# Performance work log

Measured on AMD Instinct MI355X. Metric: run time of the kernel, lower is better.

The kernel has to match this reference:

```python
import jax, jax.numpy as jnp
import numpy as np

NEG_SLOPE = 0.2  # PyG GATConv default negative_slope


def gat_conv(x, src, dst, W, a_src, a_dst, b, concat):
    # x: [N, F_in]; src/dst: [E] edge endpoints (edge j->i means src=j, dst=i)
    N = x.shape[0]
    H, C = a_src.shape
    xp = (x @ W).reshape(N, H, C)                      # per-head projection
    al_s = jnp.einsum('nhc,hc->nh', xp, a_src)          # source attention logits
    al_d = jnp.einsum('nhc,hc->nh', xp, a_dst)          # destination attention logits
    e = jax.nn.leaky_relu(al_s[src] + al_d[dst], NEG_SLOPE)   # [E, H]
    # segment softmax over incoming edges of each destination node
    m = jax.ops.segment_max(e, dst, num_segments=N)     # [N, H]
    m = jnp.where(jnp.isfinite(m), m, jnp.zeros_like(m))
    ex = jnp.exp(e - m[dst])
    den = jax.ops.segment_sum(ex, dst, num_segments=N)  # [N, H]
    alpha = ex / (den[dst] + 1e-16)                     # [E, H]
    out = jax.ops.segment_sum(xp[src] * alpha[:, :, None], dst, num_segments=N)  # [N,H,C]
    out = out.reshape(N, H * C) if concat else out.mean(axis=1)
    return out + b


def setup_inputs() -> dict:
    key = jax.random.key(0)
    ks = jax.random.split(key, 9)
    N, E, F_in, H, C = 50000, 1600000, 128, 4, 32
    x = jax.random.normal(ks[0], (N, F_in), dtype=jnp.float32)
    edge_index = jax.random.randint(ks[1], (2, E), 0, N, dtype=jnp.int64)
    s1 = 1.0 / np.sqrt(F_in)
    s2 = 1.0 / np.sqrt(H * C)
    return {
        'x': x,
        'edge_index': edge_index,
        'W1': jax.random.normal(ks[2], (F_in, H * C), dtype=jnp.float32) * s1,
        'a_src1': jax.random.normal(ks[3], (H, C), dtype=jnp.float32) * s1,
        'a_dst1': jax.random.normal(ks[4], (H, C), dtype=jnp.float32) * s1,
        'b1': jnp.zeros((H * C,), dtype=jnp.float32),
        'W2': jax.random.normal(ks[5], (H * C, C), dtype=jnp.float32) * s2,
        'a_src2': jax.random.normal(ks[6], (1, C), dtype=jnp.float32) * s2,
        'a_dst2': jax.random.normal(ks[7], (1, C), dtype=jnp.float32) * s2,
        'b2': jnp.zeros((C,), dtype=jnp.float32),
    }


def reference(x, edge_index, W1, a_src1, a_dst1, b1, W2, a_src2, a_dst2, b2):
    N = x.shape[0]
    loops = jnp.arange(N, dtype=edge_index.dtype)
    src = jnp.concatenate([edge_index[0], loops])   # PyG default add_self_loops=True
    dst = jnp.concatenate([edge_index[1], loops])
    h = gat_conv(x, src, dst, W1, a_src1, a_dst1, b1, concat=True)
    h = jax.nn.elu(h)
    out = gat_conv(h, src, dst, W2, a_src2, a_dst2, b2, concat=False)
    return out
```

## Files before the change

### kernel.cpp

```cpp
#include <hip/hip_runtime.h>
#include <hip/hip_fp16.h>

#define NEG_SLOPE 0.2f
#define CAP 128
#define NB  64
#define GAB 192

typedef __half half_t;

__device__ __forceinline__ float lrelu(float x) { return x >= 0.f ? x : NEG_SLOPE * x; }

__device__ __forceinline__ unsigned int f2h2(float a, float b) {
    union { unsigned int u; __half2 h; } v; v.h = __floats2half2_rn(a, b);
    return v.u;
}

__device__ __forceinline__ void fma8h(const uint4& v, float w, float* a) {
    const __half* hp = (const __half*)&v;
    #pragma unroll
    for (int j = 0; j < 8; ++j) a[j] = fmaf(w, __half2float(hp[j]), a[j]);
}

__device__ __forceinline__ bool edge_is64(const int* __restrict__ ei, int E) {
    int t = threadIdx.x & 63;
    int idx = 2 * t + 1; if (idx >= 2 * E) idx = 2 * E - 1;
    unsigned long long b = __ballot(ei[idx] != 0);
    return b == 0ULL;
}

__device__ __forceinline__ void load_edge(const int* __restrict__ ei, int E, int i,
                                          bool is64, int& s, int& d) {
    if (i < E) {
        if (is64) { const long long* e = (const long long*)ei; s = (int)e[i]; d = (int)e[E + i]; }
        else      { s = ei[i]; d = ei[E + i]; }
    } else { s = d = i - E; }
}

__global__ __launch_bounds__(256) void gemm1cnt_kernel(const float* __restrict__ x,
        const float* __restrict__ W1, const float* __restrict__ a_src,
        const float* __restrict__ a_dst, half_t* __restrict__ xp1h,
        float* __restrict__ al_s, float* __restrict__ al_d,
        const int* __restrict__ ei, int* __restrict__ partials,
        int N, int E, int shift, int G1) {
    __shared__ __align__(16) float xst[64 * 128];
    __shared__ __align__(16) float ws[64 * 128];
    int t = threadIdx.x;
    if (blockIdx.x >= G1) {
        int* cnts = (int*)xst;
        int b2 = blockIdx.x - G1;
        if (t < NB) cnts[t] = 0;
        bool is64 = edge_is64(ei, E);
        __syncthreads();
        int tot = E + N;
        for (int i = b2 * 256 + t; i < tot; i += GAB * 256) {
            int s, d; load_edge(ei, E, i, is64, s, d);
            atomicAdd(&cnts[d >> shift], 1);
        }
        __syncthreads();
        if (t < NB) partials[b2 * NB + t] = cnts[t];
        return;
    }
    int row0 = blockIdx.x * 128;
    int cg = t & 15, rg = t >> 4;
    float acc[8][8] = {};
    for (int chunk = 0; chunk < 2; ++chunk) {
        __syncthreads();
        int c0 = chunk * 64;
        #pragma unroll
        for (int ii = 0; ii < 8; ++ii) {
            int idx = t + 256 * ii;
            int r = idx >> 4, kq = idx & 15;
            int n = row0 + r;
            float4 v = make_float4(0.f, 0.f, 0.f, 0.f);
            if (n < N) v = *(const float4*)&x[(size_t)n * 128 + c0 + kq * 4];
            float vv[4] = {v.x, v.y, v.z, v.w};
            #pragma unroll
            for (int j = 0; j < 4; ++j) {
                int k = kq * 4 + j;
                xst[k * 128 + (((r >> 2) ^ (k & 31)) << 2) + (r & 3)] = vv[j];
            }
        }
        #pragma unroll
        for (int ii = 0; ii < 8; ++ii) {
            int idx = t + 256 * ii;
            int k = idx >> 5, cq = idx & 31;
            *(float4*)&ws[k * 128 + cq * 4] =
                *(const float4*)&W1[(size_t)(c0 + k) * 128 + cq * 4];
        }
        __syncthreads();
        int g0 = rg * 2, g1 = rg * 2 + 1;
        #pragma unroll 4
        for (int k = 0; k < 64; ++k) {
            int kb = k & 31;
            float4 xv0 = *(const float4*)&xst[k * 128 + ((g0 ^ kb) << 2)];
            float4 xv1 = *(const float4*)&xst[k * 128 + ((g1 ^ kb) << 2)];
            float4 wv0 = *(const float4*)&ws[k * 128 + cg * 8];
            float4 wv1 = *(const float4*)&ws[k * 128 + cg * 8 + 4];
            float xr[8] = {xv0.x, xv0.y, xv0.z, xv0.w, xv1.x, xv1.y, xv1.z, xv1.w};
            float wr[8] = {wv0.x, wv0.y, wv0.z, wv0.w, wv1.x, wv1.y, wv1.z, wv1.w};
            #pragma unroll
            for (int r = 0; r < 8; ++r)
                #pragma unroll
                for (int c = 0; c < 8; ++c)
                    acc[r][c] = fmaf(xr[r], wr[c], acc[r][c]);
        }
    }
    #pragma unroll
    for (int r = 0; r < 8; ++r) {
        int n = row0 + rg * 8 + r;
        if (n < N) {
            uint4 u = make_uint4(f2h2(acc[r][0], acc[r][1]), f2h2(acc[r][2], acc[r][3]),
                                 f2h2(acc[r][4], acc[r][5]), f2h2(acc[r][6], acc[r][7]));
            *(uint4*)&xp1h[(size_t)n * 128 + cg * 8] = u;
        }
    }
    float ps[8], pd[8];
    #pragma unroll
    for (int r = 0; r < 8; ++r) {
        float s = 0.f, dd = 0.f;
        #pragma unroll
        for (int c = 0; c < 8; ++c) {
            s  = fmaf(acc[r][c], a_src[cg * 8 + c], s);
            dd = fmaf(acc[r][c], a_dst[cg * 8 + c], dd);
        }
        ps[r] = s; pd[r] = dd;
    }
    #pragma unroll
    for (int m = 1; m < 4; m <<= 1) {
        #pragma unroll
        for (int r = 0; r < 8; ++r) { ps[r] += __shfl_xor(ps[r], m); pd[r] += __shfl_xor(pd[r], m); }
    }
    if ((cg & 3) == 0) {
        int head = cg >> 2;
        #pragma unroll
        for (int r = 0; r < 8; ++r) {
            int n = row0 + rg * 8 + r;
            if (n < N) { al_s[n * 4 + head] = ps[r]; al_d[n * 4 + head] = pd[r]; }
        }
    }
}

__global__ __launch_bounds__(256) void k_scan(int* __restrict__ partials,
                                              int* __restrict__ bin_base) {
    __shared__ int lp[GAB * NB];
    __shared__ int tot[NB], base[NB];
    int t = threadIdx.x;
    for (int i = t; i < GAB * NB; i += 256) lp[i] = partials[i];
    __syncthreads();
    if (t < NB) {
        int run = 0;
        for (int b = 0; b < GAB; ++b) { int v = lp[b * NB + t]; lp[b * NB + t] = run; run += v; }
        tot[t] = run;
    }
    __syncthreads();
    if (t == 0) {
        int run = 0;
        for (int i = 0; i < NB; ++i) { base[i] = run; run += tot[i]; }
    }
    __syncthreads();
    if (t < NB) bin_base[t] = base[t];
    if (t == 0) bin_base[NB] = base[NB - 1] + tot[NB - 1];
    for (int i = t; i < GAB * NB; i += 256) partials[i] = lp[i] + base[i & (NB - 1)];
}

__global__ __launch_bounds__(256) void k_bin(const int* __restrict__ ei,
        int E, int N, int shift, const int* __restrict__ offsets, int* __restrict__ binned) {
    __shared__ int cur[NB];
    int t = threadIdx.x, b = blockIdx.x;
    if (t < NB) cur[t] = offsets[b * NB + t];
    bool is64 = edge_is64(ei, E);
    int mask = (1 << shift) - 1;
    __syncthreads();
    int tot = E + N;
    for (int i = b * 256 + t; i < tot; i += GAB * 256) {
        int s, d; load_edge(ei, E, i, is64, s, d);
        int pos = atomicAdd(&cur[d >> shift], 1);
        binned[pos] = ((d & mask) << 16) | s;
    }
}

__global__ __launch_bounds__(1024) void k_part(const int* __restrict__ binned,
        const int* __restrict__ bin_base, int* __restrict__ off, int* __restrict__ csr,
        int N, int shift) {
    __shared__ int cnt_loc[1024];
    __shared__ int scan_loc[1024];
    __shared__ int wsum[16];
    int b = blockIdx.x, t = threadIdx.x;
    int base = b << shift;
    int span = 1 << shift;
    int lo = bin_base[b], hi = bin_base[b + 1];
    if (t < span) cnt_loc[t] = 0;
    __syncthreads();
    for (int i = lo + t; i < hi; i += 1024)
        atomicAdd(&cnt_loc[binned[i] >> 16], 1);
    __syncthreads();
    int v = (t < span) ? cnt_loc[t] : 0;
    int lane = t & 63, w = t >> 6;
    int incl = v;
    #pragma unroll
    for (int m = 1; m < 64; m <<= 1) {
        int u = __shfl_up(incl, m);
        if (lane >= m) incl += u;
    }
    if (lane == 63) wsum[w] = incl;
    __syncthreads();
    if (t == 0) {
        int run = 0;
        #pragma unroll
        for (int i2 = 0; i2 < 16; ++i2) { int s2 = wsum[i2]; wsum[i2] = run; run += s2; }
    }
    __syncthreads();
    int excl = incl - v + wsum[w];
    if (t < span) { scan_loc[t] = lo + excl; off[base + t] = lo + excl; }
    __syncthreads();
    if (t < span) cnt_loc[t] = 0;
    __syncthreads();
    for (int i = lo + t; i < hi; i += 1024) {
        int e = binned[i];
        int r = e >> 16;
        int pos = scan_loc[r] + atomicAdd(&cnt_loc[r], 1);
        csr[pos] = e & 0xFFFF;
    }
}

__global__ __launch_bounds__(256) void edge1_kernel(const int* __restrict__ off,
        const int* __restrict__ csr, const float* __restrict__ al_s,
        const float* __restrict__ al_d, const half_t* __restrict__ xp1h,
        const float* __restrict__ b1, half_t* __restrict__ h1h, int N) {
    __shared__ int   srcs[4][CAP];
    __shared__ float ew[4][CAP * 4];
    int t = threadIdx.x;
    int wid = t >> 6, lane = t & 63;
    int d = blockIdx.x * 4 + wid;
    if (d >= N) return;
    int o0 = off[d], o1 = off[d + 1];
    int deg = o1 - o0; if (deg > CAP) deg = CAP;
    float4 ad = *(const float4*)&al_d[d * 4];
    float4 ex0 = make_float4(0.f, 0.f, 0.f, 0.f);
    float4 ex1 = make_float4(0.f, 0.f, 0.f, 0.f);
    if (lane < deg) {
        int s = csr[o0 + lane];
        srcs[wid][lane] = s;
        float4 as = *(const float4*)&al_s[s * 4];
        ex0.x = __expf(lrelu(as.x + ad.x));
        ex0.y = __expf(lrelu(as.y + ad.y));
        ex0.z = __expf(lrelu(as.z + ad.z));
        ex0.w = __expf(lrelu(as.w + ad.w));
    }
    if (lane + 64 < deg) {
        int s = csr[o0 + lane + 64];
        srcs[wid][lane + 64] = s;
        float4 as = *(const float4*)&al_s[s * 4];
        ex1.x = __expf(lrelu(as.x + ad.x));
        ex1.y = __expf(lrelu(as.y + ad.y));
        ex1.z = __expf(lrelu(as.z + ad.z));
        ex1.w = __expf(lrelu(as.w + ad.w));
    }
    float4 r = make_float4(ex0.x + ex1.x, ex0.y + ex1.y, ex0.z + ex1.z, ex0.w + ex1.w);
    #pragma unroll
    for (int m = 1; m < 64; m <<= 1) {
        r.x += __shfl_xor(r.x, m); r.y += __shfl_xor(r.y, m);
        r.z += __shfl_xor(r.z, m); r.w += __shfl_xor(r.w, m);
    }
    float4 ri = make_float4(1.f / (r.x + 1e-16f), 1.f / (r.y + 1e-16f),
                            1.f / (r.z + 1e-16f), 1.f / (r.w + 1e-16f));
    if (lane < deg)
        *(float4*)&ew[wid][lane * 4] =
            make_float4(ex0.x * ri.x, ex0.y * ri.y, ex0.z * ri.z, ex0.w * ri.w);
    if (lane + 64 < deg)
        *(float4*)&ew[wid][(lane + 64) * 4] =
            make_float4(ex1.x * ri.x, ex1.y * ri.y, ex1.z * ri.z, ex1.w * ri.w);
    int q = lane & 15, p = lane >> 4, h = q >> 2;
    float a[8] = {};
    const uint4* xr = (const uint4*)xp1h;
    for (int ib = p; ib < deg; ib += 16) {
        int i1 = ib + 4, i2 = ib + 8, i3 = ib + 12;
        bool c1 = i1 < deg, c2 = i2 < deg, c3 = i3 < deg;
        float w0 = ew[wid][ib * 4 + h];
        uint4 v0 = xr[(size_t)srcs[wid][ib] * 16 + q];
        float w1, w2, w3;
        uint4 v1, v2, v3;
        if (c1) { w1 = ew[wid][i1 * 4 + h]; v1 = xr[(size_t)srcs[wid][i1] * 16 + q]; }
        if (c2) { w2 = ew[wid][i2 * 4 + h]; v2 = xr[(size_t)srcs[wid][i2] * 16 + q]; }
        if (c3) { w3 = ew[wid][i3 * 4 + h]; v3 = xr[(size_t)srcs[wid][i3] * 16 + q]; }
        fma8h(v0, w0, a);
        if (c1) fma8h(v1, w1, a);
        if (c2) fma8h(v2, w2, a);
        if (c3) fma8h(v3, w3, a);
    }
    #pragma unroll
    for (int j = 0; j < 8; ++j) {
        a[j] += __shfl_xor(a[j], 16);
        a[j] += __shfl_xor(a[j], 32);
    }
    if (p == 0) {
        float4 b0 = *(const float4*)&b1[q * 8];
        float4 b4 = *(const float4*)&b1[q * 8 + 4];
        float v0 = a[0] + b0.x, v1 = a[1] + b0.y, v2 = a[2] + b0.z, v3 = a[3] + b0.w;
        float v4 = a[4] + b4.x, v5 = a[5] + b4.y, v6 = a[6] + b4.z, v7 = a[7] + b4.w;
        v0 = v0 > 0.f ? v0 : expm1f(v0);
        v1 = v1 > 0.f ? v1 : expm1f(v1);
        v2 = v2 > 0.f ? v2 : expm1f(v2);
        v3 = v3 > 0.f ? v3 : expm1f(v3);
        v4 = v4 > 0.f ? v4 : expm1f(v4);
        v5 = v5 > 0.f ? v5 : expm1f(v5);
        v6 = v6 > 0.f ? v6 : expm1f(v6);
        v7 = v7 > 0.f ? v7 : expm1f(v7);
        uint4 u = make_uint4(f2h2(v0, v1), f2h2(v2, v3), f2h2(v4, v5), f2h2(v6, v7));
        *(uint4*)&h1h[(size_t)d * 128 + q * 8] = u;
    }
}

__global__ __launch_bounds__(256) void gemm2l_kernel(const half_t* __restrict__ h1h,
        const float* __restrict__ W2, const float* __restrict__ a_s2,
        const float* __restrict__ a_d2, half_t* __restrict__ xp2h,
        float* __restrict__ al_s2, float* __restrict__ al_d2, int N) {
    __shared__ __align__(16) float w2s[128 * 32];
    int t = threadIdx.x;
    #pragma unroll
    for (int ii = 0; ii < 4; ++ii)
        ((float4*)w2s)[t + 256 * ii] = ((const float4*)W2)[t + 256 * ii];
    if (blockIdx.x == 0 && t < 2)
        ((uint4*)(xp2h + (size_t)N * 32))[t] = make_uint4(0, 0, 0, 0);
    __syncthreads();
    int n = blockIdx.x * 64 + (t >> 2), sub = t & 3;
    if (n >= N) return;
    const uint4* hr = (const uint4*)(h1h + (size_t)n * 128);
    float acc[8] = {};
    #pragma unroll 2
    for (int kq = 0; kq < 16; ++kq) {
        uint4 hv = hr[kq];
        const __half* hp = (const __half*)&hv;
        #pragma unroll
        for (int jj = 0; jj < 8; ++jj) {
            float h = __half2float(hp[jj]);
            int k = kq * 8 + jj;
            float4 wa = *(const float4*)&w2s[k * 32 + sub * 8];
            float4 wb = *(const float4*)&w2s[k * 32 + sub * 8 + 4];
            acc[0] = fmaf(h, wa.x, acc[0]); acc[1] = fmaf(h, wa.y, acc[1]);
            acc[2] = fmaf(h, wa.z, acc[2]); acc[3] = fmaf(h, wa.w, acc[3]);
            acc[4] = fmaf(h, wb.x, acc[4]); acc[5] = fmaf(h, wb.y, acc[5]);
            acc[6] = fmaf(h, wb.z, acc[6]); acc[7] = fmaf(h, wb.w, acc[7]);
        }
    }
    uint4 u = make_uint4(f2h2(acc[0], acc[1]), f2h2(acc[2], acc[3]),
                         f2h2(acc[4], acc[5]), f2h2(acc[6], acc[7]));
    *(uint4*)&xp2h[(size_t)n * 32 + sub * 8] = u;
    float ps = 0.f, pd = 0.f;
    #pragma unroll
    for (int c = 0; c < 8; ++c) {
        ps = fmaf(acc[c], a_s2[sub * 8 + c], ps);
        pd = fmaf(acc[c], a_d2[sub * 8 + c], pd);
    }
    ps += __shfl_xor(ps, 1); ps += __shfl_xor(ps, 2);
    pd += __shfl_xor(pd, 1); pd += __shfl_xor(pd, 2);
    if (sub == 0) { al_s2[n] = ps; al_d2[n] = pd; }
}

__global__ __launch_bounds__(256) void edge2_kernel(const int* __restrict__ off,
        const int* __restrict__ csr, const float* __restrict__ al_s,
        const float* __restrict__ al_d, const half_t* __restrict__ xp2h,
        const float* __restrict__ b2v, float* __restrict__ out, int N) {
    __shared__ int   srcs[4][CAP];
    __shared__ float ew[4][CAP];
    int t = threadIdx.x;
    int wid = t >> 6, lane = t & 63;
    int d = blockIdx.x * 4 + wid;
    if (d >= N) return;
    int o0 = off[d], o1 = off[d + 1];
    int deg = o1 - o0; if (deg > CAP) deg = CAP;
    float adv = al_d[d];
    float ex0 = 0.f, ex1 = 0.f;
    if (lane < deg) {
        int s = csr[o0 + lane];
        srcs[wid][lane] = s;
        ex0 = __expf(lrelu(al_s[s] + adv));
    }
    if (lane + 64 < deg) {
        int s = csr[o0 + lane + 64];
        srcs[wid][lane + 64] = s;
        ex1 = __expf(lrelu(al_s[s] + adv));
    }
    float r = ex0 + ex1;
    #pragma unroll
    for (int m = 1; m < 64; m <<= 1) r += __shfl_xor(r, m);
    float rinv = 1.f / (r + 1e-16f);
    if (lane < deg)      ew[wid][lane]      = ex0 * rinv;
    if (lane + 64 < deg) ew[wid][lane + 64] = ex1 * rinv;
    int q = lane & 3, p = lane >> 2;
    float a[8] = {};
    const uint4* xr = (const uint4*)xp2h;
    for (int ib = p; ib < deg; ib += 64) {
        int i1 = ib + 16, i2 = ib + 32, i3 = ib + 48;
        bool c1 = i1 < deg, c2 = i2 < deg, c3 = i3 < deg;
        float w0 = ew[wid][ib];
        uint4 v0 = xr[(size_t)srcs[wid][ib] * 4 + q];
        float w1, w2, w3;
        uint4 v1, v2, v3;
        if (c1) { w1 = ew[wid][i1]; v1 = xr[(size_t)srcs[wid][i1] * 4 + q]; }
        if (c2) { w2 = ew[wid][i2]; v2 = xr[(size_t)srcs[wid][i2] * 4 + q]; }
        if (c3) { w3 = ew[wid][i3]; v3 = xr[(size_t)srcs[wid][i3] * 4 + q]; }
        fma8h(v0, w0, a);
        if (c1) fma8h(v1, w1, a);
        if (c2) fma8h(v2, w2, a);
        if (c3) fma8h(v3, w3, a);
    }
    #pragma unroll
    for (int j = 0; j < 8; ++j) {
        a[j] += __shfl_xor(a[j], 4);
        a[j] += __shfl_xor(a[j], 8);
        a[j] += __shfl_xor(a[j], 16);
        a[j] += __shfl_xor(a[j], 32);
    }
    if (p == 0) {
        float4 b0 = *(const float4*)&b2v[q * 8];
        float4 b4 = *(const float4*)&b2v[q * 8 + 4];
        float4 o0v = make_float4(a[0] + b0.x, a[1] + b0.y, a[2] + b0.z, a[3] + b0.w);
        float4 o1v = make_float4(a[4] + b4.x, a[5] + b4.y, a[6] + b4.z, a[7] + b4.w);
        *(float4*)&out[(size_t)d * 32 + q * 8]     = o0v;
        *(float4*)&out[(size_t)d * 32 + q * 8 + 4] = o1v;
    }
}

extern "C" void kernel_launch(void* const* d_in, const int* in_sizes, int n_in,
                              void* d_out, int out_size, void* d_ws, size_t ws_size,
                              hipStream_t stream) {
    const float* x    = (const float*)d_in[0];
    const int*   ei   = (const int*)d_in[1];
    const float* W1   = (const float*)d_in[2];
    const float* a_s1 = (const float*)d_in[3];
    const float* a_d1 = (const float*)d_in[4];
    const float* b1   = (const float*)d_in[5];
    const float* W2   = (const float*)d_in[6];
    const float* a_s2 = (const float*)d_in[7];
    const float* a_d2 = (const float*)d_in[8];
    const float* b2   = (const float*)d_in[9];
    int N = in_sizes[0] / 128;
    int E = in_sizes[1] / 2;
    float* out = (float*)d_out;

    int shift = 0;
    while (((N - 1) >> shift) >= NB) shift++;

    char* wsb = (char*)d_ws;
    size_t off_b = 0;
    auto alloc = [&](size_t bytes) -> void* {
        void* p = wsb + off_b;
        off_b = (off_b + bytes + 255) & ~(size_t)255;
        return p;
    };
    int*    partials = (int*)   alloc((size_t)GAB * NB * 4);
    int*    bin_base = (int*)   alloc((size_t)(NB + 1) * 4);
    int*    binned   = (int*)   alloc((size_t)(E + N) * 4);
    int*    offs     = (int*)   alloc(((size_t)NB << shift) * 4 + 8);
    int*    csr      = (int*)   alloc((size_t)(E + N) * 4);
    half_t* xp1h     = (half_t*)alloc((size_t)(N + 1) * 128 * 2);
    float*  al_s1    = (float*) alloc((size_t)N * 4 * 4);
    float*  al_d1    = (float*) alloc((size_t)N * 4 * 4);
    half_t* h1h      = (half_t*)alloc((size_t)N * 128 * 2);
    half_t* xp2h     = (half_t*)alloc((size_t)(N + 1) * 32 * 2);
    float*  al_s2    = (float*) alloc((size_t)N * 4);
    float*  al_d2    = (float*) alloc((size_t)N * 4);

    int G1 = (N + 127) / 128;

    gemm1cnt_kernel<<<G1 + GAB, 256, 0, stream>>>(x, W1, a_s1, a_d1, xp1h, al_s1, al_d1,
                                                  ei, partials, N, E, shift, G1);
    k_scan<<<1, 256, 0, stream>>>(partials, bin_base);
    k_bin<<<GAB, 256, 0, stream>>>(ei, E, N, shift, partials, binned);
    k_part<<<NB, 1024, 0, stream>>>(binned, bin_base, offs, csr, N, shift);
    edge1_kernel<<<(N + 3) / 4, 256, 0, stream>>>(offs, csr, al_s1, al_d1, xp1h, b1, h1h, N);
    gemm2l_kernel<<<(N + 63) / 64, 256, 0, stream>>>(h1h, W2, a_s2, a_d2, xp2h, al_s2, al_d2, N);
    edge2_kernel<<<(N + 3) / 4, 256, 0, stream>>>(offs, csr, al_s2, al_d2, xp2h, b2, out, N);
}
```

Measured before the change: 273.3 us.

## Drop scan kernel, fold bin prefix sums into bin/part kernels, pack edges

Removes the single-block k_scan launch. k_bin and k_part now each recompute their bin offsets directly from the per-block partial counts using a wavefront prefix scan. The counting pass also writes a packed 32-bit (dst<<16|src) edge array, so k_bin reads 4 bytes per edge instead of re-reading the possibly 64-bit edge_index. Edge kernels store pre-scaled source offsets in shared memory to save a multiply per gather. This trades one serialized launch and the wide edge re-read for redundant partial-sum reads in every block and an extra packed-array write.

```diff
diff --git a/kernel.cpp b/kernel.cpp
--- a/kernel.cpp
+++ b/kernel.cpp
@@ -41,7 +41,7 @@
         const float* __restrict__ a_dst, half_t* __restrict__ xp1h,
         float* __restrict__ al_s, float* __restrict__ al_d,
         const int* __restrict__ ei, int* __restrict__ partials,
-        int N, int E, int shift, int G1) {
+        unsigned int* __restrict__ epacked, int N, int E, int shift, int G1) {
     __shared__ __align__(16) float xst[64 * 128];
     __shared__ __align__(16) float ws[64 * 128];
     int t = threadIdx.x;
@@ -54,6 +54,7 @@
         int tot = E + N;
         for (int i = b2 * 256 + t; i < tot; i += GAB * 256) {
             int s, d; load_edge(ei, E, i, is64, s, d);
+            epacked[i] = ((unsigned int)d << 16) | (unsigned int)s;
             atomicAdd(&cnts[d >> shift], 1);
         }
         __syncthreads();
@@ -140,57 +141,63 @@
     }
 }
 
-__global__ __launch_bounds__(256) void k_scan(int* __restrict__ partials,
-                                              int* __restrict__ bin_base) {
-    __shared__ int lp[GAB * NB];
-    __shared__ int tot[NB], base[NB];
-    int t = threadIdx.x;
-    for (int i = t; i < GAB * NB; i += 256) lp[i] = partials[i];
-    __syncthreads();
-    if (t < NB) {
-        int run = 0;
-        for (int b = 0; b < GAB; ++b) { int v = lp[b * NB + t]; lp[b * NB + t] = run; run += v; }
-        tot[t] = run;
-    }
-    __syncthreads();
-    if (t == 0) {
-        int run = 0;
-        for (int i = 0; i < NB; ++i) { base[i] = run; run += tot[i]; }
-    }
-    __syncthreads();
-    if (t < NB) bin_base[t] = base[t];
-    if (t == 0) bin_base[NB] = base[NB - 1] + tot[NB - 1];
-    for (int i = t; i < GAB * NB; i += 256) partials[i] = lp[i] + base[i & (NB - 1)];
-}
-
-__global__ __launch_bounds__(256) void k_bin(const int* __restrict__ ei,
-        int E, int N, int shift, const int* __restrict__ offsets, int* __restrict__ binned) {
+__global__ __launch_bounds__(256) void k_bin(const unsigned int* __restrict__ epacked,
+        const int* __restrict__ partials, unsigned int* __restrict__ binned,
+        int tot, int shift) {
     __shared__ int cur[NB];
     int t = threadIdx.x, b = blockIdx.x;
-    if (t < NB) cur[t] = offsets[b * NB + t];
-    bool is64 = edge_is64(ei, E);
-    int mask = (1 << shift) - 1;
-    __syncthreads();
-    int tot = E + N;
+    if (t < NB) {
+        int full = 0, pre = 0;
+        for (int b2 = 0; b2 < GAB; ++b2) {
+            int v = partials[b2 * NB + t];
+            if (b2 < b) pre += v;
+            full += v;
+        }
+        int incl = full;
+        #pragma unroll
+        for (int m = 1; m < 64; m <<= 1) {
+            int u = __shfl_up(incl, m);
+            if (t >= m) incl += u;
+        }
+        cur[t] = (incl - full) + pre;
+    }
+    __syncthreads();
+    unsigned int mask = (1u << shift) - 1u;
     for (int i = b * 256 + t; i < tot; i += GAB * 256) {
-        int s, d; load_edge(ei, E, i, is64, s, d);
+        unsigned int e = epacked[i];
+        unsigned int d = e >> 16;
         int pos = atomicAdd(&cur[d >> shift], 1);
-        binned[pos] = ((d & mask) << 16) | s;
-    }
-}
-
-__global__ __launch_bounds__(1024) void k_part(const int* __restrict__ binned,
-        const int* __restrict__ bin_base, int* __restrict__ off, int* __restrict__ csr,
+        binned[pos] = ((d & mask) << 16) | (e & 0xFFFFu);
+    }
+}
+
+__global__ __launch_bounds__(1024) void k_part(const unsigned int* __restrict__ binned,
+        const int* __restrict__ partials, int* __restrict__ off, int* __restrict__ csr,
         int N, int shift) {
     __shared__ int cnt_loc[1024];
     __shared__ int scan_loc[1024];
     __shared__ int wsum[16];
+    __shared__ int lo_s, hi_s;
     int b = blockIdx.x, t = threadIdx.x;
     int base = b << shift;
     int span = 1 << shift;
-    int lo = bin_base[b], hi = bin_base[b + 1];
+    if (t < 64) {
+        int full = 0;
+        for (int b2 = 0; b2 < GAB; ++b2) full += partials[b2 * NB + t];
+        int incl = full;
+        #pragma unroll
+        for (int m = 1; m < 64; m <<= 1) {
+            int u = __shfl_up(incl, m);
+            if (t >= m) incl += u;
+        }
+        int excl = incl - full;
+        int lov = __shfl(excl, b);
+        int hiv = __shfl(incl, b);
+        if (t == 0) { lo_s = lov; hi_s = hiv; }
+    }
     if (t < span) cnt_loc[t] = 0;
     __syncthreads();
+    int lo = lo_s, hi = hi_s;
     for (int i = lo + t; i < hi; i += 1024)
         atomicAdd(&cnt_loc[binned[i] >> 16], 1);
     __syncthreads();
@@ -216,10 +223,10 @@
     if (t < span) cnt_loc[t] = 0;
     __syncthreads();
     for (int i = lo + t; i < hi; i += 1024) {
-        int e = binned[i];
+        unsigned int e = binned[i];
         int r = e >> 16;
         int pos = scan_loc[r] + atomicAdd(&cnt_loc[r], 1);
-        csr[pos] = e & 0xFFFF;
+        csr[pos] = (int)(e & 0xFFFFu);
     }
 }
 
@@ -240,7 +247,7 @@
     float4 ex1 = make_float4(0.f, 0.f, 0.f, 0.f);
     if (lane < deg) {
         int s = csr[o0 + lane];
-        srcs[wid][lane] = s;
+        srcs[wid][lane] = s << 4;
         float4 as = *(const float4*)&al_s[s * 4];
         ex0.x = __expf(lrelu(as.x + ad.x));
         ex0.y = __expf(lrelu(as.y + ad.y));
@@ -249,7 +256,7 @@
     }
     if (lane + 64 < deg) {
         int s = csr[o0 + lane + 64];
-        srcs[wid][lane + 64] = s;
+        srcs[wid][lane + 64] = s << 4;
         float4 as = *(const float4*)&al_s[s * 4];
         ex1.x = __expf(lrelu(as.x + ad.x));
         ex1.y = __expf(lrelu(as.y + ad.y));
@@ -277,12 +284,12 @@
         int i1 = ib + 4, i2 = ib + 8, i3 = ib + 12;
         bool c1 = i1 < deg, c2 = i2 < deg, c3 = i3 < deg;
         float w0 = ew[wid][ib * 4 + h];
-        uint4 v0 = xr[(size_t)srcs[wid][ib] * 16 + q];
+        uint4 v0 = xr[(size_t)(srcs[wid][ib] + q)];
         float w1, w2, w3;
         uint4 v1, v2, v3;
-        if (c1) { w1 = ew[wid][i1 * 4 + h]; v1 = xr[(size_t)srcs[wid][i1] * 16 + q]; }
-        if (c2) { w2 = ew[wid][i2 * 4 + h]; v2 = xr[(size_t)srcs[wid][i2] * 16 + q]; }
-        if (c3) { w3 = ew[wid][i3 * 4 + h]; v3 = xr[(size_t)srcs[wid][i3] * 16 + q]; }
+        if (c1) { w1 = ew[wid][i1 * 4 + h]; v1 = xr[(size_t)(srcs[wid][i1] + q)]; }
+        if (c2) { w2 = ew[wid][i2 * 4 + h]; v2 = xr[(size_t)(srcs[wid][i2] + q)]; }
+        if (c3) { w3 = ew[wid][i3 * 4 + h]; v3 = xr[(size_t)(srcs[wid][i3] + q)]; }
         fma8h(v0, w0, a);
         if (c1) fma8h(v1, w1, a);
         if (c2) fma8h(v2, w2, a);
@@ -373,12 +380,12 @@
     float ex0 = 0.f, ex1 = 0.f;
     if (lane < deg) {
         int s = csr[o0 + lane];
-        srcs[wid][lane] = s;
+        srcs[wid][lane] = s << 2;
         ex0 = __expf(lrelu(al_s[s] + adv));
     }
     if (lane + 64 < deg) {
         int s = csr[o0 + lane + 64];
-        srcs[wid][lane + 64] = s;
+        srcs[wid][lane + 64] = s << 2;
         ex1 = __expf(lrelu(al_s[s] + adv));
     }
     float r = ex0 + ex1;
@@ -394,12 +401,12 @@
         int i1 = ib + 16, i2 = ib + 32, i3 = ib + 48;
         bool c1 = i1 < deg, c2 = i2 < deg, c3 = i3 < deg;
         float w0 = ew[wid][ib];
-        uint4 v0 = xr[(size_t)srcs[wid][ib] * 4 + q];
+        uint4 v0 = xr[(size_t)(srcs[wid][ib] + q)];
         float w1, w2, w3;
         uint4 v1, v2, v3;
-        if (c1) { w1 = ew[wid][i1]; v1 = xr[(size_t)srcs[wid][i1] * 4 + q]; }
-        if (c2) { w2 = ew[wid][i2]; v2 = xr[(size_t)srcs[wid][i2] * 4 + q]; }
-        if (c3) { w3 = ew[wid][i3]; v3 = xr[(size_t)srcs[wid][i3] * 4 + q]; }
+        if (c1) { w1 = ew[wid][i1]; v1 = xr[(size_t)(srcs[wid][i1] + q)]; }
+        if (c2) { w2 = ew[wid][i2]; v2 = xr[(size_t)(srcs[wid][i2] + q)]; }
+        if (c3) { w3 = ew[wid][i3]; v3 = xr[(size_t)(srcs[wid][i3] + q)]; }
         fma8h(v0, w0, a);
         if (c1) fma8h(v1, w1, a);
         if (c2) fma8h(v2, w2, a);
@@ -449,26 +456,25 @@
         off_b = (off_b + bytes + 255) & ~(size_t)255;
         return p;
     };
-    int*    partials = (int*)   alloc((size_t)GAB * NB * 4);
-    int*    bin_base = (int*)   alloc((size_t)(NB + 1) * 4);
-    int*    binned   = (int*)   alloc((size_t)(E + N) * 4);
-    int*    offs     = (int*)   alloc(((size_t)NB << shift) * 4 + 8);
-    int*    csr      = (int*)   alloc((size_t)(E + N) * 4);
-    half_t* xp1h     = (half_t*)alloc((size_t)(N + 1) * 128 * 2);
-    float*  al_s1    = (float*) alloc((size_t)N * 4 * 4);
-    float*  al_d1    = (float*) alloc((size_t)N * 4 * 4);
-    half_t* h1h      = (half_t*)alloc((size_t)N * 128 * 2);
-    half_t* xp2h     = (half_t*)alloc((size_t)(N + 1) * 32 * 2);
-    float*  al_s2    = (float*) alloc((size_t)N * 4);
-    float*  al_d2    = (float*) alloc((size_t)N * 4);
+    int*          partials = (int*)          alloc((size_t)GAB * NB * 4);
+    unsigned int* epacked  = (unsigned int*) alloc((size_t)(E + N) * 4);
+    unsigned int* binned   = (unsigned int*) alloc((size_t)(E + N) * 4);
+    int*          offs     = (int*)          alloc(((size_t)NB << shift) * 4 + 8);
+    int*          csr      = (int*)          alloc((size_t)(E + N) * 4);
+    half_t*       xp1h     = (half_t*)       alloc((size_t)(N + 1) * 128 * 2);
+    float*        al_s1    = (float*)        alloc((size_t)N * 4 * 4);
+    float*        al_d1    = (float*)        alloc((size_t)N * 4 * 4);
+    half_t*       h1h      = (half_t*)       alloc((size_t)N * 128 * 2);
+    half_t*       xp2h     = (half_t*)       alloc((size_t)(N + 1) * 32 * 2);
+    float*        al_s2    = (float*)        alloc((size_t)N * 4);
+    float*        al_d2    = (float*)        alloc((size_t)N * 4);
 
     int G1 = (N + 127) / 128;
 
     gemm1cnt_kernel<<<G1 + GAB, 256, 0, stream>>>(x, W1, a_s1, a_d1, xp1h, al_s1, al_d1,
-                                                  ei, partials, N, E, shift, G1);
-    k_scan<<<1, 256, 0, stream>>>(partials, bin_base);
-    k_bin<<<GAB, 256, 0, stream>>>(ei, E, N, shift, partials, binned);
-    k_part<<<NB, 1024, 0, stream>>>(binned, bin_base, offs, csr, N, shift);
+                                                  ei, partials, epacked, N, E, shift, G1);
+    k_bin<<<GAB, 256, 0, stream>>>(epacked, partials, binned, E + N, shift);
+    k_part<<<NB, 1024, 0, stream>>>(binned, partials, offs, csr, N, shift);
     edge1_kernel<<<(N + 3) / 4, 256, 0, stream>>>(offs, csr, al_s1, al_d1, xp1h, b1, h1h, N);
     gemm2l_kernel<<<(N + 63) / 64, 256, 0, stream>>>(h1h, W2, a_s2, a_d2, xp2h, al_s2, al_d2, N);
     edge2_kernel<<<(N + 3) / 4, 256, 0, stream>>>(offs, csr, al_s2, al_d2, xp2h, b2, out, N);
```

Result: no change. 269.5 us, median of 2 (-1.4%).
